# Kernel tuning notes

Measured on AMD Instinct MI355X. Metric: run time of the kernel, lower is better.

## Reference

```python
import jax, jax.numpy as jnp
import numpy as np

TAU = 2.0
V_TH = 1.0
SURROGATE_SLOPE = 4.0


def _spike_fn(v_minus_th):
    # Heaviside forward, sigmoid surrogate gradient (straight-through).
    sur = jax.nn.sigmoid(SURROGATE_SLOPE * v_minus_th)
    hard = (v_minus_th >= 0).astype(v_minus_th.dtype)
    return jax.lax.stop_gradient(hard - sur) + sur


def _lif_scan(h):
    # h: [B, T, H] synaptic input per timestep. LIF: v += (x - v)/tau,
    # spike at v >= V_TH, soft reset v -= spike * V_TH. Membrane starts at 0.
    h_t = jnp.swapaxes(h, 0, 1)  # [T, B, H]

    def step(v, x_t):
        v = v + (x_t - v) / TAU
        s = _spike_fn(v - V_TH)
        v_next = v - s * V_TH
        return v_next, (s, v)

    v0 = jnp.zeros(h_t.shape[1:], h.dtype)
    _, (spikes, mems) = jax.lax.scan(step, v0, h_t)
    return jnp.swapaxes(spikes, 0, 1), jnp.swapaxes(mems, 0, 1)  # [B, T, H]


def setup_inputs() -> dict:
    key = jax.random.key(0)
    ks = jax.random.split(key, 4)
    B, T, D, H, O = 32, 1024, 1024, 1024, 10
    scale_in = 1.0 / np.sqrt(D)
    scale_hid = 1.0 / np.sqrt(H)
    return {
        "x": jax.random.normal(ks[0], (B, T, D), jnp.float32),
        "W_proj": jax.random.normal(ks[1], (H, D), jnp.float32) * scale_in,
        "b_proj": jnp.zeros((H,), jnp.float32),
        "W_hid": jax.random.normal(ks[2], (H, H), jnp.float32) * scale_hid,
        "b_hid": jnp.zeros((H,), jnp.float32),
        "W_out": jax.random.normal(ks[3], (O, H), jnp.float32) * scale_hid,
        "b_out": jnp.zeros((O,), jnp.float32),
    }


def reference(x, W_proj, b_proj, W_hid, b_hid, W_out, b_out):
    # dense_projection -> hidden_layer
    h = jnp.einsum("btd,hd->bth", x, W_proj) + b_proj
    h = jnp.einsum("bth,gh->btg", h, W_hid) + b_hid
    # per-timestep LIF over the time axis
    spikes, mems = _lif_scan(h)  # [B, T, H]
    # out_features != vocab_size -> classification head on time-mean of spikes
    pooled = spikes.mean(axis=1)  # [B, H]
    return pooled @ W_out.T + b_out  # [B, 10]
```

## Files before the change

### kernel.cpp

```cpp
#include <hip/hip_runtime.h>
#include <stdint.h>


typedef short v8s __attribute__((ext_vector_type(8)));
typedef _Float16 v8h __attribute__((ext_vector_type(8)));
typedef float v4f __attribute__((ext_vector_type(4)));

#define GAS __attribute__((address_space(1)))
#define LAS __attribute__((address_space(3)))

__device__ __forceinline__ unsigned short f2bf(float f) {
  unsigned int u = __float_as_uint(f);
  u += 0x7fffu + ((u >> 16) & 1u);
  return (unsigned short)(u >> 16);
}
__device__ __forceinline__ float bf2f(unsigned short h) {
  return __uint_as_float(((unsigned int)h) << 16);
}
__device__ __forceinline__ unsigned short f2h(float f) {
  union { _Float16 h; unsigned short u; } c;
  c.h = (_Float16)f;
  return c.u;
}
__device__ __forceinline__ float h2f(unsigned short u) {
  union { unsigned short u; _Float16 h; } c;
  c.u = u;
  return (float)c.h;
}

__device__ __forceinline__ void gld_lds16(const void* g, void* l) {
  __builtin_amdgcn_global_load_lds((const GAS void*)g, (LAS void*)l, 16, 0, 0);
}

__device__ __forceinline__ void split4(const float4 x, ushort4* h, ushort4* l) {
  h->x = f2bf(x.x); l->x = f2bf(x.x - bf2f(h->x));
  h->y = f2bf(x.y); l->y = f2bf(x.y - bf2f(h->y));
  h->z = f2bf(x.z); l->z = f2bf(x.z - bf2f(h->z));
  h->w = f2bf(x.w); l->w = f2bf(x.w - bf2f(h->w));
}

__global__ void __launch_bounds__(256) prep_kernel(
    const float* __restrict__ W_proj, const float* __restrict__ W_hid,
    const float* __restrict__ b_proj, const float* __restrict__ b_hid,
    unsigned short* __restrict__ WpTh, unsigned short* __restrict__ WpTl,
    unsigned short* __restrict__ Whh, unsigned short* __restrict__ Whl,
    float* __restrict__ bc) {
  __shared__ float t[32][33];
  const int blk = blockIdx.x, tid = threadIdx.x;
  if (blk < 1024) {
    const int tx = tid & 31, ty = tid >> 5;
    const int bx = blk & 31, by = blk >> 5;
    const int xc = bx * 32 + tx;
    const int yb = by * 32;
#pragma unroll
    for (int j = 0; j < 4; ++j) t[ty + 8 * j][tx] = W_proj[(size_t)(yb + ty + 8 * j) * 1024 + xc];
    __syncthreads();
    const int xo = yb + tx;
#pragma unroll
    for (int j = 0; j < 4; ++j) {
      const float v = t[tx][ty + 8 * j];
      const unsigned short h = f2bf(v);
      const size_t o = (size_t)(bx * 32 + ty + 8 * j) * 1024 + xo;
      WpTh[o] = h;
      WpTl[o] = f2bf(v - bf2f(h));
    }
  } else if (blk < 2048) {
    const int i = (blk - 1024) * 256 + tid;
    float4 v = ((const float4*)W_hid)[i];
    ushort4 h, l;
    split4(v, &h, &l);
    ((ushort4*)Whh)[i] = h;
    ((ushort4*)Whl)[i] = l;
  } else {
    const int g = (blk - 2048) * 4 + (tid >> 6);
    const int lane = tid & 63;
    const float* wr = W_hid + (size_t)g * 1024;
    float s = 0.f;
#pragma unroll
    for (int i = 0; i < 16; ++i) s += wr[lane + 64 * i] * b_proj[lane + 64 * i];
#pragma unroll
    for (int off = 32; off > 0; off >>= 1) s += __shfl_down(s, off);
    if (lane == 0) bc[g] = s + b_hid[g];
  }
}

__global__ void __launch_bounds__(256, 2)
gemm_wx(const unsigned short* __restrict__ Ah, const unsigned short* __restrict__ Al,
        const unsigned short* __restrict__ Bh, const unsigned short* __restrict__ Bl,
        const float* __restrict__ x, unsigned short* __restrict__ Xh,
        unsigned short* __restrict__ outH, unsigned short* __restrict__ outL) {
  constexpr int K = 1024, N = 1024;
  __shared__ unsigned short lds[4][64 * 32];

  const int blk = blockIdx.x, tid = threadIdx.x;

  if (blk >= 256) {
    const int i = (blk - 256) * 256 + tid;
    float4 v = ((const float4*)x)[i];
    ushort4 h;
    h.x = f2h(v.x); h.y = f2h(v.y); h.z = f2h(v.z); h.w = f2h(v.w);
    ((ushort4*)Xh)[i] = h;
    return;
  }

  const int mt = blk & 15, nt = blk >> 4;
  const int m0 = mt * 64, n0 = nt * 64;

  const int lane = tid & 63, wave = tid >> 6;
  const int wm = (wave >> 1) * 32, wn = (wave & 1) * 32;
  const int quad = lane >> 4, r = lane & 15;
  const int cs = (quad ^ ((r >> 1) & 3)) * 8;
  const int srow = tid >> 2;
  const int sslot = (tid & 3) ^ ((tid >> 3) & 3);

  const unsigned short* gAh = Ah + (size_t)(m0 + srow) * K + sslot * 8;
  const unsigned short* gAl = Al + (size_t)(m0 + srow) * K + sslot * 8;
  const unsigned short* gBh = Bh + (size_t)(n0 + srow) * K + sslot * 8;
  const unsigned short* gBl = Bl + (size_t)(n0 + srow) * K + sslot * 8;

  v4f acc[2][2];
#pragma unroll
  for (int i = 0; i < 2; ++i)
#pragma unroll
    for (int j = 0; j < 2; ++j) acc[i][j] = v4f{0.f, 0.f, 0.f, 0.f};

  for (int kt = 0; kt < K; kt += 32) {
    gld_lds16(gAh + kt, &lds[0][tid * 8]);
    gld_lds16(gAl + kt, &lds[1][tid * 8]);
    gld_lds16(gBh + kt, &lds[2][tid * 8]);
    gld_lds16(gBl + kt, &lds[3][tid * 8]);
    __syncthreads();

    v8s ah[2], al[2], bh[2], bl[2];
#pragma unroll
    for (int i = 0; i < 2; ++i) {
      ah[i] = *(const v8s*)&lds[0][(wm + i * 16 + r) * 32 + cs];
      al[i] = *(const v8s*)&lds[1][(wm + i * 16 + r) * 32 + cs];
      bh[i] = *(const v8s*)&lds[2][(wn + i * 16 + r) * 32 + cs];
      bl[i] = *(const v8s*)&lds[3][(wn + i * 16 + r) * 32 + cs];
    }
#pragma unroll
    for (int i = 0; i < 2; ++i)
#pragma unroll
      for (int j = 0; j < 2; ++j) {
        acc[i][j] = __builtin_amdgcn_mfma_f32_16x16x32_bf16(ah[i], bh[j], acc[i][j], 0, 0, 0);
        acc[i][j] = __builtin_amdgcn_mfma_f32_16x16x32_bf16(ah[i], bl[j], acc[i][j], 0, 0, 0);
        acc[i][j] = __builtin_amdgcn_mfma_f32_16x16x32_bf16(al[i], bh[j], acc[i][j], 0, 0, 0);
      }
    __syncthreads();
  }

#pragma unroll
  for (int i = 0; i < 2; ++i)
#pragma unroll
    for (int j = 0; j < 2; ++j) {
      const int gn = n0 + wn + j * 16 + r;
#pragma unroll
      for (int q2 = 0; q2 < 4; ++q2) {
        const int gm = m0 + wm + i * 16 + quad * 4 + q2;
        const float y = acc[i][j][q2];
        const unsigned short h = f2h(y);
        const size_t o = (size_t)gm * N + gn;
        outH[o] = h;
        outL[o] = f2h(y - h2f(h));
      }
    }
}

__global__ void __launch_bounds__(512, 2)
gemm_main(const unsigned short* __restrict__ Ah,
          const unsigned short* __restrict__ Bh, const unsigned short* __restrict__ Bl,
          const float* __restrict__ bias, unsigned short* __restrict__ outH, int M) {
  constexpr int K = 1024, N = 1024;
  __shared__ unsigned short lA[3][8192];
  __shared__ unsigned short lB0[3][8192];
  __shared__ unsigned short lB1[3][8192];

  const int tid = threadIdx.x;
  const int band = (M >> 8) >> 3;
  const int c = blockIdx.x & 7, idx = blockIdx.x >> 3;
  const int mt = c * band + (idx >> 2), nt = idx & 3;
  const int m0 = mt * 256, n0 = nt * 256;

  const int lane = tid & 63, wave = tid >> 6;
  const int wm = (wave >> 2) * 128, wn = (wave & 3) * 64;
  const int quad = lane >> 4, r = lane & 15;
  const int cs = (quad ^ ((r >> 1) & 3)) * 8;
  const int aoff = (wm + r) * 32 + cs;
  const int boff = (wn + r) * 32 + cs;

  const int srow = tid >> 2;
  const int sslot = (tid & 3) ^ ((tid >> 3) & 3);

  const unsigned short* gA   = Ah + (size_t)(m0 + srow) * K + sslot * 8;
  const unsigned short* gB0p = Bh + (size_t)(n0 + srow) * K + sslot * 8;
  const unsigned short* gB1p = Bl + (size_t)(n0 + srow) * K + sslot * 8;

  v4f acc[8][4];
#pragma unroll
  for (int i = 0; i < 8; ++i)
#pragma unroll
    for (int j = 0; j < 4; ++j) acc[i][j] = v4f{0.f, 0.f, 0.f, 0.f};

  unsigned short *Ac = lA[0],  *An = lA[1],  *A2 = lA[2];
  unsigned short *Bc = lB0[0], *Bn = lB0[1], *B2 = lB0[2];
  unsigned short *Cc = lB1[0], *Cn = lB1[1], *C2 = lB1[2];

  gld_lds16(gA,              &Ac[tid * 8]);
  gld_lds16(gA + 128 * K,    &Ac[4096 + tid * 8]);
  gld_lds16(gB0p,            &Bc[tid * 8]);
  gld_lds16(gB0p + 128 * K,  &Bc[4096 + tid * 8]);
  gld_lds16(gB1p,            &Cc[tid * 8]);
  gld_lds16(gB1p + 128 * K,  &Cc[4096 + tid * 8]);
  gld_lds16(gA + 32,             &An[tid * 8]);
  gld_lds16(gA + 32 + 128 * K,   &An[4096 + tid * 8]);
  gld_lds16(gB0p + 32,           &Bn[tid * 8]);
  gld_lds16(gB0p + 32 + 128 * K, &Bn[4096 + tid * 8]);
  gld_lds16(gB1p + 32,           &Cn[tid * 8]);
  gld_lds16(gB1p + 32 + 128 * K, &Cn[4096 + tid * 8]);
  asm volatile("s_waitcnt vmcnt(6)" ::: "memory");
  __builtin_amdgcn_s_barrier();
  __builtin_amdgcn_sched_barrier(0);

  v8h ah[4], bh[4];
#pragma unroll
  for (int i = 0; i < 4; ++i) ah[i] = *(const v8h*)&Ac[aoff + i * 512];
#pragma unroll
  for (int j = 0; j < 4; ++j) bh[j] = *(const v8h*)&Bc[boff + j * 512];
  __builtin_amdgcn_sched_barrier(0);

#pragma unroll 1
  for (int t = 0; t < 32; ++t) {
    const int kp = (t + 2) * 32;
    const bool pf = (t < 30);
    v8h bl[4], ah2[4], anx[4], bnx[4];

#pragma unroll
    for (int j = 0; j < 4; ++j) bl[j] = *(const v8h*)&Cc[boff + j * 512];
    if (pf) {
      gld_lds16(gA + kp,           &A2[tid * 8]);
      gld_lds16(gA + kp + 128 * K, &A2[4096 + tid * 8]);
    }
    __builtin_amdgcn_sched_barrier(0);
    __builtin_amdgcn_s_barrier();
    asm volatile("s_waitcnt lgkmcnt(4)" ::: "memory");
    __builtin_amdgcn_sched_barrier(0);
    __builtin_amdgcn_s_setprio(1);
#pragma unroll
    for (int i = 0; i < 4; ++i)
#pragma unroll
      for (int j = 0; j < 4; ++j)
        acc[i][j] = __builtin_amdgcn_mfma_f32_16x16x32_f16(ah[i], bh[j], acc[i][j], 0, 0, 0);
    __builtin_amdgcn_s_setprio(0);
    __builtin_amdgcn_sched_barrier(0);
    __builtin_amdgcn_s_barrier();

#pragma unroll
    for (int i = 0; i < 4; ++i) ah2[i] = *(const v8h*)&Ac[aoff + (4 + i) * 512];
    if (pf) {
      gld_lds16(gB0p + kp,           &B2[tid * 8]);
      gld_lds16(gB0p + kp + 128 * K, &B2[4096 + tid * 8]);
    }
    __builtin_amdgcn_sched_barrier(0);
    __builtin_amdgcn_s_barrier();
    asm volatile("s_waitcnt vmcnt(4) lgkmcnt(4)" ::: "memory");
    __builtin_amdgcn_sched_barrier(0);
    __builtin_amdgcn_s_setprio(1);
#pragma unroll
    for (int i = 0; i < 4; ++i)
#pragma unroll
      for (int j = 0; j < 4; ++j)
        acc[i][j] = __builtin_amdgcn_mfma_f32_16x16x32_f16(ah[i], bl[j], acc[i][j], 0, 0, 0);
    __builtin_amdgcn_s_setprio(0);
    __builtin_amdgcn_sched_barrier(0);
    __builtin_amdgcn_s_barrier();

#pragma unroll
    for (int i = 0; i < 4; ++i) anx[i] = *(const v8h*)&An[aoff + i * 512];
#pragma unroll
    for (int j = 0; j < 4; ++j) bnx[j] = *(const v8h*)&Bn[boff + j * 512];
    if (pf) {
      gld_lds16(gB1p + kp,           &C2[tid * 8]);
      gld_lds16(gB1p + kp + 128 * K, &C2[4096 + tid * 8]);
    }
    __builtin_amdgcn_sched_barrier(0);
    __builtin_amdgcn_s_barrier();
    asm volatile("s_waitcnt lgkmcnt(8)" ::: "memory");
    __builtin_amdgcn_sched_barrier(0);
    __builtin_amdgcn_s_setprio(1);
#pragma unroll
    for (int i = 0; i < 4; ++i)
#pragma unroll
      for (int j = 0; j < 4; ++j)
        acc[4 + i][j] = __builtin_amdgcn_mfma_f32_16x16x32_f16(ah2[i], bh[j], acc[4 + i][j], 0, 0, 0);
    __builtin_amdgcn_s_setprio(0);
    __builtin_amdgcn_sched_barrier(0);
    __builtin_amdgcn_s_barrier();

    __builtin_amdgcn_s_setprio(1);
#pragma unroll
    for (int i = 0; i < 4; ++i)
#pragma unroll
      for (int j = 0; j < 4; ++j)
        acc[4 + i][j] = __builtin_amdgcn_mfma_f32_16x16x32_f16(ah2[i], bl[j], acc[4 + i][j], 0, 0, 0);
    __builtin_amdgcn_s_setprio(0);
    __builtin_amdgcn_sched_barrier(0);
    __builtin_amdgcn_s_barrier();

    unsigned short* tp;
    tp = Ac; Ac = An; An = A2; A2 = tp;
    tp = Bc; Bc = Bn; Bn = B2; B2 = tp;
    tp = Cc; Cc = Cn; Cn = C2; C2 = tp;
#pragma unroll
    for (int i = 0; i < 4; ++i) { ah[i] = anx[i]; bh[i] = bnx[i]; }
  }

  float bv[4];
#pragma unroll
  for (int j = 0; j < 4; ++j) bv[j] = bias[n0 + wn + j * 16 + r];
#pragma unroll
  for (int i = 0; i < 8; ++i)
#pragma unroll
    for (int j = 0; j < 4; ++j) {
      const int gn = n0 + wn + j * 16 + r;
#pragma unroll
      for (int q2 = 0; q2 < 4; ++q2) {
        const int gm = m0 + wm + i * 16 + quad * 4 + q2;
        outH[(size_t)gm * N + gn] = f2h(acc[i][j][q2] + bv[j]);
      }
    }
}

__global__ void __launch_bounds__(256) lif_part_kernel(const unsigned short* __restrict__ y2,
                                                       float* __restrict__ part) {
  const int gid = blockIdx.x * 256 + threadIdx.x;
  const int chunk = gid >> 13;
  const int c4 = (gid & 8191) << 2;
  const unsigned short* p = y2 + ((size_t)(c4 >> 10) << 20) + (c4 & 1023);
  const int t0 = chunk << 7;
  float v0 = 0.f, v1 = 0.f, v2 = 0.f, v3 = 0.f;
  if (chunk) {
    const unsigned short* pw = p + (size_t)(t0 - 32) * 1024;
    for (int b = 0; b < 32; b += 16) {
      ushort4 x[16];
#pragma unroll
      for (int i = 0; i < 16; ++i) x[i] = *(const ushort4*)&pw[(size_t)(b + i) * 1024];
#pragma unroll
      for (int i = 0; i < 16; ++i) {
        v0 += (h2f(x[i].x) - v0) * 0.5f; if (v0 >= 1.0f) v0 -= 1.0f;
        v1 += (h2f(x[i].y) - v1) * 0.5f; if (v1 >= 1.0f) v1 -= 1.0f;
        v2 += (h2f(x[i].z) - v2) * 0.5f; if (v2 >= 1.0f) v2 -= 1.0f;
        v3 += (h2f(x[i].w) - v3) * 0.5f; if (v3 >= 1.0f) v3 -= 1.0f;
      }
    }
  }
  float c0 = 0.f, c1 = 0.f, c2 = 0.f, c3 = 0.f;
  const unsigned short* pm = p + (size_t)t0 * 1024;
  for (int b = 0; b < 128; b += 16) {
    ushort4 x[16];
#pragma unroll
    for (int i = 0; i < 16; ++i) x[i] = *(const ushort4*)&pm[(size_t)(b + i) * 1024];
#pragma unroll
    for (int i = 0; i < 16; ++i) {
      float s;
      v0 += (h2f(x[i].x) - v0) * 0.5f; s = (v0 >= 1.0f) ? 1.0f : 0.0f; c0 += s; v0 -= s;
      v1 += (h2f(x[i].y) - v1) * 0.5f; s = (v1 >= 1.0f) ? 1.0f : 0.0f; c1 += s; v1 -= s;
      v2 += (h2f(x[i].z) - v2) * 0.5f; s = (v2 >= 1.0f) ? 1.0f : 0.0f; c2 += s; v2 -= s;
      v3 += (h2f(x[i].w) - v3) * 0.5f; s = (v3 >= 1.0f) ? 1.0f : 0.0f; c3 += s; v3 -= s;
    }
  }
  float4 o; o.x = c0; o.y = c1; o.z = c2; o.w = c3;
  *(float4*)&part[(size_t)chunk * 32768 + c4] = o;
}

__global__ void __launch_bounds__(64) head_kernel(const float* __restrict__ part,
                                                  const float* __restrict__ W_out,
                                                  const float* __restrict__ b_out,
                                                  float* __restrict__ out) {
  int blk = blockIdx.x;
  int b = blk / 10, o = blk % 10;
  int lane = threadIdx.x;
  const float* wr = W_out + o * 1024;
  float s = 0.f;
#pragma unroll
  for (int i = 0; i < 16; ++i) {
    const int ch = b * 1024 + lane + 64 * i;
    float p = 0.f;
#pragma unroll
    for (int c = 0; c < 8; ++c) p += part[c * 32768 + ch];
    s += p * wr[lane + 64 * i];
  }
#pragma unroll
  for (int off = 32; off > 0; off >>= 1) s += __shfl_down(s, off);
  if (lane == 0) out[b * 10 + o] = s * (1.0f / 1024.0f) + b_out[o];
}

extern "C" void kernel_launch(void* const* d_in, const int* in_sizes, int n_in,
                              void* d_out, int out_size, void* d_ws, size_t ws_size,
                              hipStream_t stream) {
  const float* x      = (const float*)d_in[0];
  const float* W_proj = (const float*)d_in[1];
  const float* b_proj = (const float*)d_in[2];
  const float* W_hid  = (const float*)d_in[3];
  const float* b_hid  = (const float*)d_in[4];
  const float* W_out  = (const float*)d_in[5];
  const float* b_out  = (const float*)d_in[6];
  float* out = (float*)d_out;

  const int M = 32768;

  char* ws = (char*)d_ws;
  unsigned short* Xh   = (unsigned short*)(ws);
  unsigned short* Y2   = (unsigned short*)(ws + 67108864);
  char* base = ws + 134217728;
  unsigned short* WpTh = (unsigned short*)(base);
  unsigned short* WpTl = (unsigned short*)(base + 2097152);
  unsigned short* Whh  = (unsigned short*)(base + 4194304);
  unsigned short* Whl  = (unsigned short*)(base + 6291456);
  unsigned short* Wch  = (unsigned short*)(base + 8388608);
  unsigned short* Wcl  = (unsigned short*)(base + 10485760);
  float*           bc  = (float*)(base + 12582912);
  float*          part = (float*)(base + 12582912 + 65536);

  prep_kernel<<<2304, 256, 0, stream>>>(W_proj, W_hid, b_proj, b_hid,
                                        WpTh, WpTl, Whh, Whl, bc);
  gemm_wx<<<33024, 256, 0, stream>>>(Whh, Whl, WpTh, WpTl, x, Xh, Wch, Wcl);
  gemm_main<<<512, 512, 0, stream>>>(Xh, Wch, Wcl, bc, Y2, M);
  lif_part_kernel<<<256, 256, 0, stream>>>(Y2, part);
  head_kernel<<<320, 64, 0, stream>>>(part, W_out, b_out, out);
}
```

Measured before the change: 341.7 us.

## Drop low-half weight correction in main GEMM and fuse LIF scan with head

Removes the hi/lo split of the combined weight matrix, so the main GEMM runs one f16 MFMA pass instead of two and loads one B tile stream instead of two. The pipeline is restructured to match, and the LDS footprint shrinks. The LIF partial-chunk kernel and the head kernel are merged into one sequential-scan kernel that reduces into the output with atomics, and the output is zeroed in the prep kernel. This drops a launch and the warm-up recomputation, at the cost of less parallelism in the scan and lower precision in the combined weights, which could flip spikes near threshold.

```diff
diff --git a/kernel.cpp b/kernel.cpp
--- a/kernel.cpp
+++ b/kernel.cpp
@@ -8,6 +8,7 @@
 
 #define GAS __attribute__((address_space(1)))
 #define LAS __attribute__((address_space(3)))
+#define SB __builtin_amdgcn_sched_barrier(0)
 
 __device__ __forceinline__ unsigned short f2bf(float f) {
   unsigned int u = __float_as_uint(f);
@@ -44,7 +45,7 @@
     const float* __restrict__ b_proj, const float* __restrict__ b_hid,
     unsigned short* __restrict__ WpTh, unsigned short* __restrict__ WpTl,
     unsigned short* __restrict__ Whh, unsigned short* __restrict__ Whl,
-    float* __restrict__ bc) {
+    float* __restrict__ bc, float* __restrict__ out) {
   __shared__ float t[32][33];
   const int blk = blockIdx.x, tid = threadIdx.x;
   if (blk < 1024) {
@@ -71,7 +72,7 @@
     split4(v, &h, &l);
     ((ushort4*)Whh)[i] = h;
     ((ushort4*)Whl)[i] = l;
-  } else {
+  } else if (blk < 2304) {
     const int g = (blk - 2048) * 4 + (tid >> 6);
     const int lane = tid & 63;
     const float* wr = W_hid + (size_t)g * 1024;
@@ -81,6 +82,8 @@
 #pragma unroll
     for (int off = 32; off > 0; off >>= 1) s += __shfl_down(s, off);
     if (lane == 0) bc[g] = s + b_hid[g];
+  } else {
+    if (tid < 320) out[tid] = 0.f;
   }
 }
 
@@ -88,7 +91,7 @@
 gemm_wx(const unsigned short* __restrict__ Ah, const unsigned short* __restrict__ Al,
         const unsigned short* __restrict__ Bh, const unsigned short* __restrict__ Bl,
         const float* __restrict__ x, unsigned short* __restrict__ Xh,
-        unsigned short* __restrict__ outH, unsigned short* __restrict__ outL) {
+        unsigned short* __restrict__ outH) {
   constexpr int K = 1024, N = 1024;
   __shared__ unsigned short lds[4][64 * 32];
 
@@ -158,23 +161,18 @@
 #pragma unroll
       for (int q2 = 0; q2 < 4; ++q2) {
         const int gm = m0 + wm + i * 16 + quad * 4 + q2;
-        const float y = acc[i][j][q2];
-        const unsigned short h = f2h(y);
-        const size_t o = (size_t)gm * N + gn;
-        outH[o] = h;
-        outL[o] = f2h(y - h2f(h));
+        outH[(size_t)gm * N + gn] = f2h(acc[i][j][q2]);
       }
     }
 }
 
 __global__ void __launch_bounds__(512, 2)
 gemm_main(const unsigned short* __restrict__ Ah,
-          const unsigned short* __restrict__ Bh, const unsigned short* __restrict__ Bl,
+          const unsigned short* __restrict__ Bh,
           const float* __restrict__ bias, unsigned short* __restrict__ outH, int M) {
   constexpr int K = 1024, N = 1024;
   __shared__ unsigned short lA[3][8192];
-  __shared__ unsigned short lB0[3][8192];
-  __shared__ unsigned short lB1[3][8192];
+  __shared__ unsigned short lB[3][8192];
 
   const int tid = threadIdx.x;
   const int band = (M >> 8) >> 3;
@@ -192,9 +190,8 @@
   const int srow = tid >> 2;
   const int sslot = (tid & 3) ^ ((tid >> 3) & 3);
 
-  const unsigned short* gA   = Ah + (size_t)(m0 + srow) * K + sslot * 8;
-  const unsigned short* gB0p = Bh + (size_t)(n0 + srow) * K + sslot * 8;
-  const unsigned short* gB1p = Bl + (size_t)(n0 + srow) * K + sslot * 8;
+  const unsigned short* gA = Ah + (size_t)(m0 + srow) * K + sslot * 8;
+  const unsigned short* gB = Bh + (size_t)(n0 + srow) * K + sslot * 8;
 
   v4f acc[8][4];
 #pragma unroll
@@ -202,49 +199,44 @@
 #pragma unroll
     for (int j = 0; j < 4; ++j) acc[i][j] = v4f{0.f, 0.f, 0.f, 0.f};
 
-  unsigned short *Ac = lA[0],  *An = lA[1],  *A2 = lA[2];
-  unsigned short *Bc = lB0[0], *Bn = lB0[1], *B2 = lB0[2];
-  unsigned short *Cc = lB1[0], *Cn = lB1[1], *C2 = lB1[2];
-
-  gld_lds16(gA,              &Ac[tid * 8]);
-  gld_lds16(gA + 128 * K,    &Ac[4096 + tid * 8]);
-  gld_lds16(gB0p,            &Bc[tid * 8]);
-  gld_lds16(gB0p + 128 * K,  &Bc[4096 + tid * 8]);
-  gld_lds16(gB1p,            &Cc[tid * 8]);
-  gld_lds16(gB1p + 128 * K,  &Cc[4096 + tid * 8]);
-  gld_lds16(gA + 32,             &An[tid * 8]);
-  gld_lds16(gA + 32 + 128 * K,   &An[4096 + tid * 8]);
-  gld_lds16(gB0p + 32,           &Bn[tid * 8]);
-  gld_lds16(gB0p + 32 + 128 * K, &Bn[4096 + tid * 8]);
-  gld_lds16(gB1p + 32,           &Cn[tid * 8]);
-  gld_lds16(gB1p + 32 + 128 * K, &Cn[4096 + tid * 8]);
-  asm volatile("s_waitcnt vmcnt(6)" ::: "memory");
+  unsigned short *Ac = lA[0], *An = lA[1], *A2 = lA[2];
+  unsigned short *Bc = lB[0], *Bn = lB[1], *B2 = lB[2];
+
+  gld_lds16(gA,             &Ac[tid * 8]);
+  gld_lds16(gA + 128 * K,   &Ac[4096 + tid * 8]);
+  gld_lds16(gB,             &Bc[tid * 8]);
+  gld_lds16(gB + 128 * K,   &Bc[4096 + tid * 8]);
+  gld_lds16(gA + 32,            &An[tid * 8]);
+  gld_lds16(gA + 32 + 128 * K,  &An[4096 + tid * 8]);
+  gld_lds16(gB + 32,            &Bn[tid * 8]);
+  gld_lds16(gB + 32 + 128 * K,  &Bn[4096 + tid * 8]);
+  asm volatile("s_waitcnt vmcnt(4)" ::: "memory");
   __builtin_amdgcn_s_barrier();
-  __builtin_amdgcn_sched_barrier(0);
+  SB;
 
   v8h ah[4], bh[4];
 #pragma unroll
   for (int i = 0; i < 4; ++i) ah[i] = *(const v8h*)&Ac[aoff + i * 512];
 #pragma unroll
   for (int j = 0; j < 4; ++j) bh[j] = *(const v8h*)&Bc[boff + j * 512];
-  __builtin_amdgcn_sched_barrier(0);
+  SB;
 
 #pragma unroll 1
   for (int t = 0; t < 32; ++t) {
     const int kp = (t + 2) * 32;
     const bool pf = (t < 30);
-    v8h bl[4], ah2[4], anx[4], bnx[4];
-
-#pragma unroll
-    for (int j = 0; j < 4; ++j) bl[j] = *(const v8h*)&Cc[boff + j * 512];
+    v8h ah2[4], anx[4], bnx[4];
+
+#pragma unroll
+    for (int i = 0; i < 4; ++i) ah2[i] = *(const v8h*)&Ac[aoff + (4 + i) * 512];
     if (pf) {
       gld_lds16(gA + kp,           &A2[tid * 8]);
       gld_lds16(gA + kp + 128 * K, &A2[4096 + tid * 8]);
     }
-    __builtin_amdgcn_sched_barrier(0);
+    SB;
     __builtin_amdgcn_s_barrier();
     asm volatile("s_waitcnt lgkmcnt(4)" ::: "memory");
-    __builtin_amdgcn_sched_barrier(0);
+    SB;
     __builtin_amdgcn_s_setprio(1);
 #pragma unroll
     for (int i = 0; i < 4; ++i)
@@ -252,41 +244,22 @@
       for (int j = 0; j < 4; ++j)
         acc[i][j] = __builtin_amdgcn_mfma_f32_16x16x32_f16(ah[i], bh[j], acc[i][j], 0, 0, 0);
     __builtin_amdgcn_s_setprio(0);
-    __builtin_amdgcn_sched_barrier(0);
+    SB;
     __builtin_amdgcn_s_barrier();
 
-#pragma unroll
-    for (int i = 0; i < 4; ++i) ah2[i] = *(const v8h*)&Ac[aoff + (4 + i) * 512];
     if (pf) {
-      gld_lds16(gB0p + kp,           &B2[tid * 8]);
-      gld_lds16(gB0p + kp + 128 * K, &B2[4096 + tid * 8]);
-    }
-    __builtin_amdgcn_sched_barrier(0);
+      gld_lds16(gB + kp,           &B2[tid * 8]);
+      gld_lds16(gB + kp + 128 * K, &B2[4096 + tid * 8]);
+    }
+    SB;
     __builtin_amdgcn_s_barrier();
-    asm volatile("s_waitcnt vmcnt(4) lgkmcnt(4)" ::: "memory");
-    __builtin_amdgcn_sched_barrier(0);
-    __builtin_amdgcn_s_setprio(1);
-#pragma unroll
-    for (int i = 0; i < 4; ++i)
-#pragma unroll
-      for (int j = 0; j < 4; ++j)
-        acc[i][j] = __builtin_amdgcn_mfma_f32_16x16x32_f16(ah[i], bl[j], acc[i][j], 0, 0, 0);
-    __builtin_amdgcn_s_setprio(0);
-    __builtin_amdgcn_sched_barrier(0);
-    __builtin_amdgcn_s_barrier();
-
+    if (pf) asm volatile("s_waitcnt vmcnt(4) lgkmcnt(0)" ::: "memory");
+    else    asm volatile("s_waitcnt vmcnt(0) lgkmcnt(0)" ::: "memory");
+    SB;
 #pragma unroll
     for (int i = 0; i < 4; ++i) anx[i] = *(const v8h*)&An[aoff + i * 512];
 #pragma unroll
     for (int j = 0; j < 4; ++j) bnx[j] = *(const v8h*)&Bn[boff + j * 512];
-    if (pf) {
-      gld_lds16(gB1p + kp,           &C2[tid * 8]);
-      gld_lds16(gB1p + kp + 128 * K, &C2[4096 + tid * 8]);
-    }
-    __builtin_amdgcn_sched_barrier(0);
-    __builtin_amdgcn_s_barrier();
-    asm volatile("s_waitcnt lgkmcnt(8)" ::: "memory");
-    __builtin_amdgcn_sched_barrier(0);
     __builtin_amdgcn_s_setprio(1);
 #pragma unroll
     for (int i = 0; i < 4; ++i)
@@ -294,23 +267,12 @@
       for (int j = 0; j < 4; ++j)
         acc[4 + i][j] = __builtin_amdgcn_mfma_f32_16x16x32_f16(ah2[i], bh[j], acc[4 + i][j], 0, 0, 0);
     __builtin_amdgcn_s_setprio(0);
-    __builtin_amdgcn_sched_barrier(0);
-    __builtin_amdgcn_s_barrier();
-
-    __builtin_amdgcn_s_setprio(1);
-#pragma unroll
-    for (int i = 0; i < 4; ++i)
-#pragma unroll
-      for (int j = 0; j < 4; ++j)
-        acc[4 + i][j] = __builtin_amdgcn_mfma_f32_16x16x32_f16(ah2[i], bl[j], acc[4 + i][j], 0, 0, 0);
-    __builtin_amdgcn_s_setprio(0);
-    __builtin_amdgcn_sched_barrier(0);
+    SB;
     __builtin_amdgcn_s_barrier();
 
     unsigned short* tp;
     tp = Ac; Ac = An; An = A2; A2 = tp;
     tp = Bc; Bc = Bn; Bn = B2; B2 = tp;
-    tp = Cc; Cc = Cn; Cn = C2; C2 = tp;
 #pragma unroll
     for (int i = 0; i < 4; ++i) { ah[i] = anx[i]; bh[i] = bnx[i]; }
   }
@@ -331,68 +293,48 @@
     }
 }
 
-__global__ void __launch_bounds__(256) lif_part_kernel(const unsigned short* __restrict__ y2,
-                                                       float* __restrict__ part) {
-  const int gid = blockIdx.x * 256 + threadIdx.x;
-  const int chunk = gid >> 13;
-  const int c4 = (gid & 8191) << 2;
-  const unsigned short* p = y2 + ((size_t)(c4 >> 10) << 20) + (c4 & 1023);
-  const int t0 = chunk << 7;
-  float v0 = 0.f, v1 = 0.f, v2 = 0.f, v3 = 0.f;
-  if (chunk) {
-    const unsigned short* pw = p + (size_t)(t0 - 32) * 1024;
-    for (int b = 0; b < 32; b += 16) {
-      ushort4 x[16];
-#pragma unroll
-      for (int i = 0; i < 16; ++i) x[i] = *(const ushort4*)&pw[(size_t)(b + i) * 1024];
-#pragma unroll
-      for (int i = 0; i < 16; ++i) {
-        v0 += (h2f(x[i].x) - v0) * 0.5f; if (v0 >= 1.0f) v0 -= 1.0f;
-        v1 += (h2f(x[i].y) - v1) * 0.5f; if (v1 >= 1.0f) v1 -= 1.0f;
-        v2 += (h2f(x[i].z) - v2) * 0.5f; if (v2 >= 1.0f) v2 -= 1.0f;
-        v3 += (h2f(x[i].w) - v3) * 0.5f; if (v3 >= 1.0f) v3 -= 1.0f;
-      }
-    }
-  }
-  float c0 = 0.f, c1 = 0.f, c2 = 0.f, c3 = 0.f;
-  const unsigned short* pm = p + (size_t)t0 * 1024;
-  for (int b = 0; b < 128; b += 16) {
-    ushort4 x[16];
-#pragma unroll
-    for (int i = 0; i < 16; ++i) x[i] = *(const ushort4*)&pm[(size_t)(b + i) * 1024];
-#pragma unroll
-    for (int i = 0; i < 16; ++i) {
-      float s;
-      v0 += (h2f(x[i].x) - v0) * 0.5f; s = (v0 >= 1.0f) ? 1.0f : 0.0f; c0 += s; v0 -= s;
-      v1 += (h2f(x[i].y) - v1) * 0.5f; s = (v1 >= 1.0f) ? 1.0f : 0.0f; c1 += s; v1 -= s;
-      v2 += (h2f(x[i].z) - v2) * 0.5f; s = (v2 >= 1.0f) ? 1.0f : 0.0f; c2 += s; v2 -= s;
-      v3 += (h2f(x[i].w) - v3) * 0.5f; s = (v3 >= 1.0f) ? 1.0f : 0.0f; c3 += s; v3 -= s;
-    }
-  }
-  float4 o; o.x = c0; o.y = c1; o.z = c2; o.w = c3;
-  *(float4*)&part[(size_t)chunk * 32768 + c4] = o;
-}
-
-__global__ void __launch_bounds__(64) head_kernel(const float* __restrict__ part,
-                                                  const float* __restrict__ W_out,
-                                                  const float* __restrict__ b_out,
-                                                  float* __restrict__ out) {
-  int blk = blockIdx.x;
-  int b = blk / 10, o = blk % 10;
-  int lane = threadIdx.x;
-  const float* wr = W_out + o * 1024;
-  float s = 0.f;
-#pragma unroll
-  for (int i = 0; i < 16; ++i) {
-    const int ch = b * 1024 + lane + 64 * i;
-    float p = 0.f;
-#pragma unroll
-    for (int c = 0; c < 8; ++c) p += part[c * 32768 + ch];
-    s += p * wr[lane + 64 * i];
-  }
-#pragma unroll
-  for (int off = 32; off > 0; off >>= 1) s += __shfl_down(s, off);
-  if (lane == 0) out[b * 10 + o] = s * (1.0f / 1024.0f) + b_out[o];
+__global__ void __launch_bounds__(128) lif_head_kernel(
+    const unsigned short* __restrict__ y2, const float* __restrict__ W_out,
+    const float* __restrict__ b_out, float* __restrict__ out) {
+  const int blk = blockIdx.x;
+  const int b = blk >> 3, q = blk & 7;
+  const int ch = q * 128 + threadIdx.x;
+  const unsigned short* p = y2 + ((size_t)b << 20) + ch;
+
+  float v = 0.f, cnt = 0.f;
+  for (int tb = 0; tb < 32; ++tb) {
+    unsigned short xr[32];
+#pragma unroll
+    for (int i = 0; i < 32; ++i) xr[i] = p[(size_t)(tb * 32 + i) * 1024];
+#pragma unroll
+    for (int i = 0; i < 32; ++i) {
+      v += (h2f(xr[i]) - v) * 0.5f;
+      float s = (v >= 1.0f) ? 1.0f : 0.0f;
+      cnt += s;
+      v -= s;
+    }
+  }
+
+  const float pooled = cnt * (1.0f / 1024.0f);
+  float pp[10];
+#pragma unroll
+  for (int o = 0; o < 10; ++o) pp[o] = pooled * W_out[o * 1024 + ch];
+#pragma unroll
+  for (int o = 0; o < 10; ++o)
+#pragma unroll
+    for (int off = 32; off > 0; off >>= 1) pp[o] += __shfl_down(pp[o], off);
+
+  __shared__ float ls[2][10];
+  const int lane = threadIdx.x & 63, wv = threadIdx.x >> 6;
+  if (lane == 0)
+#pragma unroll
+    for (int o = 0; o < 10; ++o) ls[wv][o] = pp[o];
+  __syncthreads();
+  if (threadIdx.x < 10) {
+    float s = ls[0][threadIdx.x] + ls[1][threadIdx.x];
+    if (q == 0) s += b_out[threadIdx.x];
+    atomicAdd(&out[b * 10 + threadIdx.x], s);
+  }
 }
 
 extern "C" void kernel_launch(void* const* d_in, const int* in_sizes, int n_in,
@@ -418,14 +360,11 @@
   unsigned short* Whh  = (unsigned short*)(base + 4194304);
   unsigned short* Whl  = (unsigned short*)(base + 6291456);
   unsigned short* Wch  = (unsigned short*)(base + 8388608);
-  unsigned short* Wcl  = (unsigned short*)(base + 10485760);
-  float*           bc  = (float*)(base + 12582912);
-  float*          part = (float*)(base + 12582912 + 65536);
-
-  prep_kernel<<<2304, 256, 0, stream>>>(W_proj, W_hid, b_proj, b_hid,
-                                        WpTh, WpTl, Whh, Whl, bc);
-  gemm_wx<<<33024, 256, 0, stream>>>(Whh, Whl, WpTh, WpTl, x, Xh, Wch, Wcl);
-  gemm_main<<<512, 512, 0, stream>>>(Xh, Wch, Wcl, bc, Y2, M);
-  lif_part_kernel<<<256, 256, 0, stream>>>(Y2, part);
-  head_kernel<<<320, 64, 0, stream>>>(part, W_out, b_out, out);
-}
+  float*           bc  = (float*)(base + 10485760);
+
+  prep_kernel<<<2305, 256, 0, stream>>>(W_proj, W_hid, b_proj, b_hid,
+                                        WpTh, WpTl, Whh, Whl, bc, out);
+  gemm_wx<<<33024, 256, 0, stream>>>(Whh, Whl, WpTh, WpTl, x, Xh, Wch);
+  gemm_main<<<512, 512, 0, stream>>>(Xh, Wch, bc, Y2, M);
+  lif_head_kernel<<<256, 128, 0, stream>>>(Y2, W_out, b_out, out);
+}
```

Result: faster. 315.5 us (-7.7%).
